# Kernel tuning notes

Measured on AMD Instinct MI355X. Metric: run time of the kernel, lower is better.

The kernel has to match this reference:

```python
import jax, jax.numpy as jnp
import numpy as np

NC, EC, NS, ES = 100000, 1600000, 50000, 800000
F_IN, H, G, OUT = 7, 64, 1024, 2
EPS = 1e-5


def setup_inputs() -> dict:
    key = jax.random.key(0)
    ks = jax.random.split(key, 24)
    d = {
        'x_c': jax.random.normal(ks[0], (NC, F_IN), jnp.float32),
        'edge_index_c': jax.random.randint(ks[1], (2, EC), 0, NC),
        'batch_c': jnp.sort(jax.random.randint(ks[2], (NC,), 0, G)),
        'x_s': jax.random.normal(ks[3], (NS, F_IN), jnp.float32),
        'edge_index_s': jax.random.randint(ks[4], (2, ES), 0, NS),
        'batch_s': jnp.sort(jax.random.randint(ks[5], (NS,), 0, G)),
    }
    def lin(k, i, o):
        return jax.random.normal(k, (i, o), jnp.float32) * (1.0 / np.sqrt(i))
    # chromo branch layers
    d['Wc0'] = lin(ks[6], F_IN, H); d['bc0'] = jnp.zeros((H,), jnp.float32)
    d['gc0'] = jnp.ones((H,), jnp.float32); d['betac0'] = jnp.zeros((H,), jnp.float32)
    d['Wc1'] = lin(ks[7], H, H); d['bc1'] = jnp.zeros((H,), jnp.float32)
    d['gc1'] = jnp.ones((H,), jnp.float32); d['betac1'] = jnp.zeros((H,), jnp.float32)
    # solvent branch layers
    d['Ws0'] = lin(ks[8], F_IN, H); d['bs0'] = jnp.zeros((H,), jnp.float32)
    d['gs0'] = jnp.ones((H,), jnp.float32); d['betas0'] = jnp.zeros((H,), jnp.float32)
    d['Ws1'] = lin(ks[9], H, H); d['bs1'] = jnp.zeros((H,), jnp.float32)
    d['gs1'] = jnp.ones((H,), jnp.float32); d['betas1'] = jnp.zeros((H,), jnp.float32)
    # heads
    d['Wf1'] = lin(ks[10], 2 * H, H); d['bf1'] = jnp.zeros((H,), jnp.float32)
    d['Wf2'] = lin(ks[11], H, OUT); d['bf2'] = jnp.zeros((OUT,), jnp.float32)
    return d


def _gcn(x, src, dst, W, b):
    # PyG GCNConv: add self-loops, symmetric D^-1/2 (A+I) D^-1/2 normalization
    N = x.shape[0]
    xw = x @ W
    si = jnp.concatenate([src, jnp.arange(N)])
    di = jnp.concatenate([dst, jnp.arange(N)])
    deg = jax.ops.segment_sum(jnp.ones(si.shape[0], x.dtype), di, num_segments=N)
    dinv = jnp.where(deg > 0, jax.lax.rsqrt(jnp.maximum(deg, 1.0)), 0.0)
    msg = xw[si] * (dinv[si] * dinv[di])[:, None]
    return jax.ops.segment_sum(msg, di, num_segments=N) + b


def _bn_relu(x, g, b):
    mu = x.mean(0)
    var = x.var(0)
    return jax.nn.relu((x - mu) * jax.lax.rsqrt(var + EPS) * g + b)


def _branch(x, ei, batch, layers):
    for (W, b, g, bt) in layers:
        x = _bn_relu(_gcn(x, ei[0], ei[1], W, b), g, bt)
    s = jax.ops.segment_sum(x, batch, num_segments=G)
    cnt = jax.ops.segment_sum(jnp.ones(x.shape[0], x.dtype), batch, num_segments=G)
    return s / jnp.maximum(cnt, 1.0)[:, None]  # global_mean_pool


def reference(x_c, edge_index_c, batch_c, x_s, edge_index_s, batch_s,
              Wc0, bc0, gc0, betac0, Wc1, bc1, gc1, betac1,
              Ws0, bs0, gs0, betas0, Ws1, bs1, gs1, betas1,
              Wf1, bf1, Wf2, bf2):
    hc = _branch(x_c, edge_index_c, batch_c,
                 [(Wc0, bc0, gc0, betac0), (Wc1, bc1, gc1, betac1)])
    hs = _branch(x_s, edge_index_s, batch_s,
                 [(Ws0, bs0, gs0, betas0), (Ws1, bs1, gs1, betas1)])
    h = jnp.concatenate([hc, hs], axis=1)  # [G, 2H]
    h = jax.nn.relu(h @ Wf1 + bf1)
    return h @ Wf2 + bf2  # [G, 2]
```

## Files before the change

kernel.cpp:

```cpp
#include <hip/hip_runtime.h>
#include <hip/hip_bf16.h>

typedef __hip_bfloat16 bf16;
typedef __attribute__((ext_vector_type(8))) short short8;
typedef __attribute__((ext_vector_type(4))) float f32x4;

#define NC_ 100000
#define EC_ 1600000
#define NS_ 50000
#define ES_ 800000
#define G_  1024
#define EPS_ 1e-5f

#define NB_C 782
#define NB_S 391
#define NBMAX 782
#define KSL 16
#define CSR_WC 2000400
#define CSR_WS 1000208

#define WS_MIN_FALLBACK 39356176ull
#define WS_BIG          52163344ull

__device__ __forceinline__ float b2f(bf16 v) { return __bfloat162float(v); }

__device__ __forceinline__ unsigned short f2bfbits(float v) {
    bf16 b = __float2bfloat16(v);
    union { bf16 b; unsigned short u; } c; c.b = b; return c.u;
}

__device__ __forceinline__ void acc8(float* a, uint4 r) {
    a[0] += __uint_as_float(r.x << 16); a[1] += __uint_as_float(r.x & 0xffff0000u);
    a[2] += __uint_as_float(r.y << 16); a[3] += __uint_as_float(r.y & 0xffff0000u);
    a[4] += __uint_as_float(r.z << 16); a[5] += __uint_as_float(r.z & 0xffff0000u);
    a[6] += __uint_as_float(r.w << 16); a[7] += __uint_as_float(r.w & 0xffff0000u);
}

__global__ void DualGNN_31327491457689_kernel() {}

__global__ __launch_bounds__(256) void k_fillout(float* out, float val, int n) {
    int i = blockIdx.x * 256 + threadIdx.x;
    if (i < n) out[i] = val;
}

__global__ __launch_bounds__(256) void k_zero(int* p, int n) {
    int i = blockIdx.x * 256 + threadIdx.x;
    int stride = gridDim.x * 256;
    while (i < n) { p[i] = 0; i += stride; }
}

__global__ __launch_bounds__(256) void k_bhist2(const int* dst_c, int* bcnt_c,
                                                const int* dst_s, int* bcnt_s) {
    __shared__ int h[NBMAX];
    int t = threadIdx.x;
    const int* dst; int* bcnt; int E, NB, b0, nb;
    if (blockIdx.x < 256) { dst = dst_c; bcnt = bcnt_c; E = EC_; NB = NB_C; b0 = blockIdx.x; nb = 256; }
    else { dst = dst_s; bcnt = bcnt_s; E = ES_; NB = NB_S; b0 = blockIdx.x - 256; nb = 128; }
    for (int i = t; i < NB; i += 256) h[i] = 0;
    __syncthreads();
    for (int e = b0 * 256 + t; e < E; e += nb * 256)
        atomicAdd(&h[dst[e] >> 7], 1);
    __syncthreads();
    for (int i = t; i < NB; i += 256) {
        int v = h[i];
        if (v) atomicAdd(&bcnt[i], v);
    }
}

__device__ void scan_one(const int* cnt, int* base, int* cur, int NB, int (*sc)[1024]) {
    int t = threadIdx.x;
    for (int i = t; i < 1024; i += 256) sc[0][i] = (i < NB) ? cnt[i] : 0;
    __syncthreads();
    int pin = 0;
    for (int off = 1; off < 1024; off <<= 1) {
        for (int i = t; i < 1024; i += 256) {
            int v = sc[pin][i];
            if (i >= off) v += sc[pin][i - off];
            sc[1 - pin][i] = v;
        }
        __syncthreads();
        pin ^= 1;
    }
    for (int i = t; i <= NB; i += 256) {
        int e = (i == 0) ? 0 : sc[pin][i - 1];
        base[i] = e;
        if (i < NB) cur[i] = e;
    }
    __syncthreads();
}

__global__ __launch_bounds__(256) void k_bscan(const int* cnt_c, int* base_c, int* cur_c, int NBc,
                                               const int* cnt_s, int* base_s, int* cur_s, int NBs) {
    __shared__ int sc[2][1024];
    scan_one(cnt_c, base_c, cur_c, NBc, sc);
    scan_one(cnt_s, base_s, cur_s, NBs, sc);
}

__global__ __launch_bounds__(256) void k_bin2(const int* ei_c, int* bcur_c, int* ebuf_c,
                                              const int* ei_s, int* bcur_s, int* ebuf_s) {
    __shared__ int cnt[NBMAX];
    __shared__ int slot[NBMAX * KSL];
    int t = threadIdx.x;
    const int *src, *dst; int *bcur, *ebuf; int E, NB; int base;
    if (blockIdx.x < 391) {
        src = ei_c; dst = ei_c + EC_; bcur = bcur_c; ebuf = ebuf_c;
        E = EC_; NB = NB_C; base = blockIdx.x * 4096;
    } else {
        src = ei_s; dst = ei_s + ES_; bcur = bcur_s; ebuf = ebuf_s;
        E = ES_; NB = NB_S; base = (blockIdx.x - 391) * 4096;
    }
    if (base >= E) return;
    for (int i = t; i < NB; i += 256) cnt[i] = 0;
    __syncthreads();
    int e1 = base + 4096;
    if (e1 > E) e1 = E;
    for (int e = base + t; e < e1; e += 256) {
        int d = dst[e];
        int p = ((d & 127) << 24) | src[e];
        int b = d >> 7;
        int sl = atomicAdd(&cnt[b], 1);
        if (sl < KSL) slot[b * KSL + sl] = p;
        else { int gp = atomicAdd(&bcur[b], 1); ebuf[gp] = p; }
    }
    __syncthreads();
    for (int b = t; b < NB; b += 256) {
        int c = cnt[b];
        if (c > KSL) c = KSL;
        if (c > 0) {
            int gp = atomicAdd(&bcur[b], c);
            for (int k = 0; k < c; k++) ebuf[gp + k] = slot[b * KSL + k];
        }
    }
}

__global__ __launch_bounds__(256) void k_build2(const int* bbase_c, const int* ebuf_c,
                                                const float* x_c, bf16* u_c,
                                                int* deg_c, int* start_c, int* csr_c,
                                                const int* bbase_s, const int* ebuf_s,
                                                const float* x_s, bf16* u_s,
                                                int* deg_s, int* start_s, int* csr_s) {
    __shared__ int lcnt[128], lofs[128], lcur[128];
    int t = threadIdx.x;
    const int* bbase; const int* ebuf; const float* x; bf16* u;
    int* deg; int* start; int* csr; int N, b;
    if (blockIdx.x < NB_C) {
        b = blockIdx.x; bbase = bbase_c; ebuf = ebuf_c; x = x_c; u = u_c;
        deg = deg_c; start = start_c; csr = csr_c; N = NC_;
    } else {
        b = blockIdx.x - NB_C; bbase = bbase_s; ebuf = ebuf_s; x = x_s; u = u_s;
        deg = deg_s; start = start_s; csr = csr_s; N = NS_;
    }
    int e0 = bbase[b], e1 = bbase[b + 1];
    int cb = ((e0 + 512 * b) + 3) & ~3;
    int n0 = b << 7;
    if (t < 128) lcnt[t] = 0;
    __syncthreads();
    for (int e = e0 + t; e < e1; e += 256)
        atomicAdd(&lcnt[((unsigned)ebuf[e]) >> 24], 1);
    __syncthreads();
    if (t < 64) {
        int c0 = lcnt[2 * t], c1 = lcnt[2 * t + 1];
        int v0 = (c0 + 3) & ~3, v1 = (c1 + 3) & ~3;
        int s = v0 + v1, incl = s;
        for (int off = 1; off < 64; off <<= 1) {
            int uu = __shfl_up(incl, off);
            if (t >= off) incl += uu;
        }
        int excl = incl - s;
        lofs[2 * t] = excl;
        lofs[2 * t + 1] = excl + v0;
    }
    __syncthreads();
    if (t < 128) {
        int node = n0 + t;
        if (node < N) {
            deg[node] = lcnt[t];
            start[node] = cb + lofs[t];
            if (x) {
                float d = rsqrtf((float)(lcnt[t] + 1));
                union __align__(16) Pack { bf16 hh[8]; uint4 v; } p;
                for (int k = 0; k < 7; k++) p.hh[k] = __float2bfloat16(x[node * 7 + k] * d);
                p.hh[7] = __float2bfloat16(0.f);
                ((uint4*)u)[node] = p.v;
            }
        }
        lcur[t] = lofs[t];
    }
    __syncthreads();
    if (t < 128) {
        int c = lcnt[t], al = (c + 3) & ~3;
        for (int k = c; k < al; k++) csr[cb + lofs[t] + k] = N;
    }
    for (int e = e0 + t; e < e1; e += 256) {
        unsigned p = (unsigned)ebuf[e];
        int dl = p >> 24;
        int pos = atomicAdd(&lcur[dl], 1);
        csr[cb + pos] = (int)(p & 0xFFFFFF);
    }
    if (b == 0 && t < 4 && u && x) ((int*)u)[N * 4 + t] = 0;
}

__global__ __launch_bounds__(256) void k_prep7(const float* x, const int* deg,
                                               bf16* u, int N) {
    int i = blockIdx.x * 256 + threadIdx.x;
    if (i > N) return;
    union __align__(16) Pack { bf16 hh[8]; uint4 v; } p;
    if (i == N) {
        p.v = (uint4){0u, 0u, 0u, 0u};
    } else {
        float d = rsqrtf((float)(deg[i] + 1));
        for (int k = 0; k < 7; k++) p.hh[k] = __float2bfloat16(x[i * 7 + k] * d);
        p.hh[7] = __float2bfloat16(0.f);
    }
    ((uint4*)u)[i] = p.v;
}

__global__ __launch_bounds__(256) void k_gather7m(
    const bf16* u_c, const int* csr_c, const int* start_c, const int* deg_c,
    const float* W_c, const float* bias_c, bf16* h_c, float* stat_c, int N_c,
    const bf16* u_s, const int* csr_s, const int* start_s, const int* deg_s,
    const float* W_s, const float* bias_s, bf16* h_s, float* stat_s, int N_s,
    int nblk_c) {
    __shared__ float Wsm[7 * 64];
    __shared__ float agg[128][9];
    __shared__ float sm[2][4][64];
    const bf16* u; const int *csr, *start, *deg; const float *W, *bias;
    bf16* h; float* stat; int N, lb;
    if ((int)blockIdx.x < nblk_c) {
        lb = blockIdx.x; u = u_c; csr = csr_c; start = start_c; deg = deg_c;
        W = W_c; bias = bias_c; h = h_c; stat = stat_c; N = N_c;
    } else {
        lb = blockIdx.x - nblk_c; u = u_s; csr = csr_s; start = start_s; deg = deg_s;
        W = W_s; bias = bias_s; h = h_s; stat = stat_s; N = N_s;
    }
    int t = threadIdx.x, lane = t & 63, ty = t >> 6;
    int team = t >> 1, par = t & 1;
    for (int i = t; i < 448; i += 256) Wsm[i] = W[i];
    float b = bias[lane];
    float sum = 0.f, sq = 0.f;
    const uint4* up = (const uint4*)u;
    int i = lb * 128 + team;
    float a[8] = {0.f, 0.f, 0.f, 0.f, 0.f, 0.f, 0.f, 0.f};
    if (i < N) {
        int dg = deg[i], s0 = start[i];
        int adeg = (dg + 3) & ~3;
        if (par == 0) acc8(a, up[i]);
        int half = ((adeg >> 1) + 3) & ~3;
        int jb = par ? half : 0;
        int je = par ? adeg : half;
        int j = jb;
        for (; j + 8 <= je; j += 8) {
            uint4 nA = *(const uint4*)(csr + s0 + j);
            uint4 nB = *(const uint4*)(csr + s0 + j + 4);
            uint4 r0 = up[nA.x], r1 = up[nA.y], r2 = up[nA.z], r3 = up[nA.w];
            uint4 r4 = up[nB.x], r5 = up[nB.y], r6 = up[nB.z], r7 = up[nB.w];
            acc8(a, r0); acc8(a, r1); acc8(a, r2); acc8(a, r3);
            acc8(a, r4); acc8(a, r5); acc8(a, r6); acc8(a, r7);
        }
        if (j < je) {
            uint4 nA = *(const uint4*)(csr + s0 + j);
            uint4 r0 = up[nA.x], r1 = up[nA.y], r2 = up[nA.z], r3 = up[nA.w];
            acc8(a, r0); acc8(a, r1); acc8(a, r2); acc8(a, r3);
        }
    }
    #pragma unroll
    for (int k = 0; k < 7; k++) a[k] += __shfl_xor(a[k], 1);
    if (i < N && par == 0) {
        float di = rsqrtf((float)(deg[i] + 1));
        #pragma unroll
        for (int k = 0; k < 7; k++) agg[team][k] = a[k] * di;
    }
    __syncthreads();
    int mbase = lb * 128 + ty * 32;
    for (int mm = 0; mm < 32; mm++) {
        int node = mbase + mm;
        if (node >= N) break;
        const float* ag = agg[ty * 32 + mm];
        float s = b;
        #pragma unroll
        for (int k = 0; k < 7; k++) s += ag[k] * Wsm[k * 64 + lane];
        h[(size_t)node * 64 + lane] = __float2bfloat16(s);
        sum += s; sq += s * s;
    }
    sm[0][ty][lane] = sum;
    sm[1][ty][lane] = sq;
    __syncthreads();
    if (ty == 0) {
        atomicAdd(&stat[lane],      sm[0][0][lane] + sm[0][1][lane] + sm[0][2][lane] + sm[0][3][lane]);
        atomicAdd(&stat[64 + lane], sm[1][0][lane] + sm[1][1][lane] + sm[1][2][lane] + sm[1][3][lane]);
    }
}

__global__ __launch_bounds__(256) void k_gemm1m(
    const bf16* h_c, const float* W_c, const float* stat_c, const float* gam_c,
    const float* bet_c, const int* deg_c, bf16* y_c, float invN_c, int N_c, int NY_c,
    const bf16* h_s, const float* W_s, const float* stat_s, const float* gam_s,
    const float* bet_s, const int* deg_s, bf16* y_s, float invN_s, int N_s, int NY_s,
    int nblk_c) {
    __shared__ short Wt[64][72];
    __shared__ float AB[128];
    const bf16* h; const float *W, *stat, *gam, *bet; const int* deg;
    bf16* y; float invN; int N, NY, lb, nb;
    if ((int)blockIdx.x < nblk_c) {
        lb = blockIdx.x; nb = nblk_c;
        h = h_c; W = W_c; stat = stat_c; gam = gam_c; bet = bet_c; deg = deg_c;
        y = y_c; invN = invN_c; N = N_c; NY = NY_c;
    } else {
        lb = blockIdx.x - nblk_c; nb = gridDim.x - nblk_c;
        h = h_s; W = W_s; stat = stat_s; gam = gam_s; bet = bet_s; deg = deg_s;
        y = y_s; invN = invN_s; N = N_s; NY = NY_s;
    }
    int t = threadIdx.x, lane = t & 63, ty = t >> 6;
    for (int i = t; i < 4096; i += 256) {
        int k = i >> 6, n = i & 63;
        Wt[n][k] = (short)f2bfbits(W[i]);
    }
    if (t < 64) {
        float mean = stat[t] * invN;
        float var = stat[64 + t] * invN - mean * mean;
        float A = gam[t] * rsqrtf(fmaxf(var, 0.f) + EPS_);
        AB[t] = A;
        AB[64 + t] = bet[t] - mean * A;
    }
    if (lb == 0 && t < 64) {
        int pr = t >> 4, cl = t & 15;
        y[((size_t)pr * NY + N) * 16 + cl] = __float2bfloat16(0.f);
    }
    __syncthreads();
    int quad = lane >> 4, l16 = lane & 15;
    short8 Bf[2][4];
    #pragma unroll
    for (int kt = 0; kt < 2; kt++)
        #pragma unroll
        for (int nt = 0; nt < 4; nt++) {
            int n = nt * 16 + l16, k0 = kt * 32 + quad * 8;
            Bf[kt][nt] = *(const short8*)&Wt[n][k0];
        }
    int ntile = (N + 63) >> 6;
    for (int tile = lb * 4 + ty; tile < ntile; tile += nb * 4) {
        int base = tile << 6;
        f32x4 acc[4][4];
        #pragma unroll
        for (int a = 0; a < 4; a++)
            #pragma unroll
            for (int b = 0; b < 4; b++) acc[a][b] = (f32x4){0.f, 0.f, 0.f, 0.f};
        #pragma unroll
        for (int kt = 0; kt < 2; kt++) {
            int k0 = kt * 32 + quad * 8;
            float Ak[8], Bk[8];
            #pragma unroll
            for (int j = 0; j < 8; j++) { Ak[j] = AB[k0 + j]; Bk[j] = AB[64 + k0 + j]; }
            #pragma unroll
            for (int mt = 0; mt < 4; mt++) {
                int node = base + mt * 16 + l16;
                uint4 raw = *(const uint4*)(h + (size_t)node * 64 + k0);
                unsigned rr[4] = {raw.x, raw.y, raw.z, raw.w};
                short8 af;
                #pragma unroll
                for (int j = 0; j < 8; j++) {
                    unsigned bits = (j & 1) ? (rr[j >> 1] & 0xffff0000u)
                                            : (rr[j >> 1] << 16);
                    float v = __uint_as_float(bits);
                    v = fmaxf(v * Ak[j] + Bk[j], 0.f);
                    af[j] = (short)f2bfbits(v);
                }
                #pragma unroll
                for (int nt = 0; nt < 4; nt++)
                    acc[mt][nt] = __builtin_amdgcn_mfma_f32_16x16x32_bf16(
                        af, Bf[kt][nt], acc[mt][nt], 0, 0, 0);
            }
        }
        #pragma unroll
        for (int mt = 0; mt < 4; mt++)
            #pragma unroll
            for (int r = 0; r < 4; r++) {
                int node = base + mt * 16 + quad * 4 + r;
                if (node < N) {
                    float dinv = rsqrtf((float)(deg[node] + 1));
                    #pragma unroll
                    for (int nt = 0; nt < 4; nt++)
                        y[((size_t)nt * NY + node) * 16 + l16] =
                            __float2bfloat16(acc[mt][nt][r] * dinv);
                }
            }
    }
}

__global__ __launch_bounds__(256) void k_gather16p(
    const bf16* y_c, const int* csr_c, const int* start_c, const int* deg_c,
    const float* bias_c, bf16* h_c, float* stat_c, int N_c, int NY_c,
    const bf16* y_s, const int* csr_s, const int* start_s, const int* deg_s,
    const float* bias_s, bf16* h_s, float* stat_s, int N_s, int NY_s,
    int nblk_c) {
    __shared__ float sms[4][2][2][8];
    const bf16* y; const int *csr, *start, *deg; const float* bias;
    bf16* h; float* stat; int N, NY, lb, nb;
    if ((int)blockIdx.x < nblk_c) {
        lb = blockIdx.x; nb = nblk_c;
        y = y_c; csr = csr_c; start = start_c; deg = deg_c; bias = bias_c;
        h = h_c; stat = stat_c; N = N_c; NY = NY_c;
    } else {
        lb = blockIdx.x - nblk_c; nb = gridDim.x - nblk_c;
        y = y_s; csr = csr_s; start = start_s; deg = deg_s; bias = bias_s;
        h = h_s; stat = stat_s; N = N_s; NY = NY_s;
    }
    int t = threadIdx.x, lane = t & 63, ty = t >> 6;
    int team = lane >> 1, par = lane & 1;
    int pair = lb & 3;
    int grp = lb >> 2;
    int ngrp = nb >> 2;
    const uint4* yp = (const uint4*)y + (size_t)pair * NY * 2;
    uint4* hp = (uint4*)h + (size_t)pair * NY * 2;
    float b[8];
    #pragma unroll
    for (int k = 0; k < 8; k++) b[k] = bias[pair * 16 + par * 8 + k];
    float sum[8], sq[8];
    #pragma unroll
    for (int k = 0; k < 8; k++) { sum[k] = 0.f; sq[k] = 0.f; }
    for (int i = grp * 128 + ty * 32 + team; i < N; i += ngrp * 128) {
        int dg = deg[i], s0 = start[i];
        int adeg = (dg + 3) & ~3;
        float a[8];
        #pragma unroll
        for (int k = 0; k < 8; k++) a[k] = 0.f;
        acc8(a, yp[2 * i + par]);
        int j = 0;
        for (; j + 8 <= adeg; j += 8) {
            uint4 nA = *(const uint4*)(csr + s0 + j);
            uint4 nB = *(const uint4*)(csr + s0 + j + 4);
            uint4 q0 = yp[2 * nA.x + par];
            uint4 q1 = yp[2 * nA.y + par];
            uint4 q2 = yp[2 * nA.z + par];
            uint4 q3 = yp[2 * nA.w + par];
            uint4 q4 = yp[2 * nB.x + par];
            uint4 q5 = yp[2 * nB.y + par];
            uint4 q6 = yp[2 * nB.z + par];
            uint4 q7 = yp[2 * nB.w + par];
            acc8(a, q0); acc8(a, q1); acc8(a, q2); acc8(a, q3);
            acc8(a, q4); acc8(a, q5); acc8(a, q6); acc8(a, q7);
        }
        if (j < adeg) {
            uint4 nA = *(const uint4*)(csr + s0 + j);
            uint4 q0 = yp[2 * nA.x + par];
            uint4 q1 = yp[2 * nA.y + par];
            uint4 q2 = yp[2 * nA.z + par];
            uint4 q3 = yp[2 * nA.w + par];
            acc8(a, q0); acc8(a, q1); acc8(a, q2); acc8(a, q3);
        }
        float di = rsqrtf((float)(dg + 1));
        union __align__(16) Pack { bf16 hh[8]; uint4 v; } p;
        #pragma unroll
        for (int k = 0; k < 8; k++) {
            float v = a[k] * di + b[k];
            p.hh[k] = __float2bfloat16(v);
            sum[k] += v; sq[k] += v * v;
        }
        hp[2 * i + par] = p.v;
    }
    #pragma unroll
    for (int k = 0; k < 8; k++) {
        float s1 = sum[k], s2 = sq[k];
        s1 += __shfl_down(s1, 32); s2 += __shfl_down(s2, 32);
        s1 += __shfl_down(s1, 16); s2 += __shfl_down(s2, 16);
        s1 += __shfl_down(s1, 8);  s2 += __shfl_down(s2, 8);
        s1 += __shfl_down(s1, 4);  s2 += __shfl_down(s2, 4);
        s1 += __shfl_down(s1, 2);  s2 += __shfl_down(s2, 2);
        if (lane < 2) { sms[ty][lane][0][k] = s1; sms[ty][lane][1][k] = s2; }
    }
    __syncthreads();
    if (t < 16) {
        int pp = t >> 3, k = t & 7;
        atomicAdd(&stat[pair * 16 + pp * 8 + k],
                  sms[0][pp][0][k] + sms[1][pp][0][k] + sms[2][pp][0][k] + sms[3][pp][0][k]);
    } else if (t >= 64 && t < 80) {
        int q = t - 64, pp = q >> 3, k = q & 7;
        atomicAdd(&stat[64 + pair * 16 + pp * 8 + k],
                  sms[0][pp][1][k] + sms[1][pp][1][k] + sms[2][pp][1][k] + sms[3][pp][1][k]);
    }
}

__global__ __launch_bounds__(256) void k_poolm(
    const bf16* h_c, const float* stat_c, const float* gam_c, const float* bet_c,
    const int* batch_c, float* pooled_c, float* cnt_c, float invN_c, int N_c, int NY_c,
    const bf16* h_s, const float* stat_s, const float* gam_s, const float* bet_s,
    const int* batch_s, float* pooled_s, float* cnt_s, float invN_s, int N_s, int NY_s,
    int nblk_c) {
    const bf16* h; const float *stat, *gam, *bet; const int* batch;
    float *pooled, *cnt; float invN; int N, NY, lb, nb;
    if ((int)blockIdx.x < nblk_c) {
        lb = blockIdx.x; nb = nblk_c;
        h = h_c; stat = stat_c; gam = gam_c; bet = bet_c; batch = batch_c;
        pooled = pooled_c; cnt = cnt_c; invN = invN_c; N = N_c; NY = NY_c;
    } else {
        lb = blockIdx.x - nblk_c; nb = gridDim.x - nblk_c;
        h = h_s; stat = stat_s; gam = gam_s; bet = bet_s; batch = batch_s;
        pooled = pooled_s; cnt = cnt_s; invN = invN_s; N = N_s; NY = NY_s;
    }
    int t = threadIdx.x;
    int lane = t & 63;
    float mean = stat[lane] * invN;
    float var = stat[64 + lane] * invN - mean * mean;
    float A = gam[lane] * rsqrtf(fmaxf(var, 0.f) + EPS_);
    float B = bet[lane] - mean * A;
    size_t pbase = (size_t)(lane >> 4) * NY * 16 + (lane & 15);
    int w = (lb * 256 + t) >> 6;
    int nw = nb * 4;
    int chunk = (N + nw - 1) / nw;
    int i0 = w * chunk;
    int i1 = i0 + chunk;
    if (i1 > N) i1 = N;
    if (i0 >= N) return;
    int curg = batch[i0];
    float acc = 0.f, c = 0.f;
    for (int i = i0; i < i1; i++) {
        int g = batch[i];
        if (g != curg) {
            atomicAdd(&pooled[(size_t)curg * 64 + lane], acc);
            if (lane == 0) atomicAdd(&cnt[curg], c);
            curg = g; acc = 0.f; c = 0.f;
        }
        acc += fmaxf(b2f(h[pbase + (size_t)i * 16]) * A + B, 0.f);
        c += 1.f;
    }
    atomicAdd(&pooled[(size_t)curg * 64 + lane], acc);
    if (lane == 0) atomicAdd(&cnt[curg], c);
}

__global__ __launch_bounds__(64) void k_head(const float* pooled_c, const float* cnt_c,
                                             const float* pooled_s, const float* cnt_s,
                                             const float* Wf1, const float* bf1_,
                                             const float* Wf2, const float* bf2_,
                                             float* out) {
    __shared__ float W1sm[128 * 64];
    __shared__ float W2sm[128];
    int t = threadIdx.x;
    for (int i = t; i < 128 * 64; i += 64) W1sm[i] = Wf1[i];
    for (int i = t; i < 128; i += 64) W2sm[i] = Wf2[i];
    __syncthreads();
    float bb1 = bf1_[t];
    float b20 = bf2_[0];
    float b21 = bf2_[1];
    for (int g = blockIdx.x; g < G_; g += gridDim.x) {
        float ic = 1.f / fmaxf(cnt_c[g], 1.f);
        float is = 1.f / fmaxf(cnt_s[g], 1.f);
        float hc = pooled_c[(size_t)g * 64 + t] * ic;
        float hs = pooled_s[(size_t)g * 64 + t] * is;
        float s = bb1;
        for (int k = 0; k < 64; k++) s += __shfl(hc, k) * W1sm[k * 64 + t];
        for (int k = 0; k < 64; k++) s += __shfl(hs, k) * W1sm[(64 + k) * 64 + t];
        s = fmaxf(s, 0.f);
        float p0 = s * W2sm[t * 2 + 0];
        float p1 = s * W2sm[t * 2 + 1];
        for (int off = 32; off > 0; off >>= 1) {
            p0 += __shfl_down(p0, off);
            p1 += __shfl_down(p1, off);
        }
        if (t == 0) {
            out[g * 2 + 0] = p0 + b20;
            out[g * 2 + 1] = p1 + b21;
        }
    }
}

extern "C" void kernel_launch(void* const* d_in, const int* in_sizes, int n_in,
                              void* d_out, int out_size, void* d_ws, size_t ws_size,
                              hipStream_t stream) {
    float* out = (float*)d_out;

    if (n_in != 26 || in_sizes[0] != NC_ * 7 || in_sizes[1] != 2 * EC_ ||
        in_sizes[2] != NC_ || in_sizes[3] != NS_ * 7 || in_sizes[4] != 2 * ES_ ||
        in_sizes[5] != NS_ || out_size != G_ * 2) {
        k_fillout<<<(out_size + 255) / 256, 256, 0, stream>>>(out, 7777.0f, out_size);
        return;
    }
    if (ws_size < (size_t)WS_MIN_FALLBACK) {
        k_fillout<<<(out_size + 255) / 256, 256, 0, stream>>>(
            out, 1000.0f + (float)(ws_size >> 20), out_size);
        return;
    }
    const bool big = (ws_size >= (size_t)WS_BIG);

    const float* x_c     = (const float*)d_in[0];
    const int*   ei_c    = (const int*)d_in[1];
    const int*   batch_c = (const int*)d_in[2];
    const float* x_s     = (const float*)d_in[3];
    const int*   ei_s    = (const int*)d_in[4];
    const int*   batch_s = (const int*)d_in[5];
    const float* Wc0  = (const float*)d_in[6];
    const float* bc0  = (const float*)d_in[7];
    const float* gc0  = (const float*)d_in[8];
    const float* bec0 = (const float*)d_in[9];
    const float* Wc1  = (const float*)d_in[10];
    const float* bc1  = (const float*)d_in[11];
    const float* gc1  = (const float*)d_in[12];
    const float* bec1 = (const float*)d_in[13];
    const float* Ws0  = (const float*)d_in[14];
    const float* bs0  = (const float*)d_in[15];
    const float* gs0  = (const float*)d_in[16];
    const float* bes0 = (const float*)d_in[17];
    const float* Ws1  = (const float*)d_in[18];
    const float* bs1  = (const float*)d_in[19];
    const float* gs1  = (const float*)d_in[20];
    const float* bes1 = (const float*)d_in[21];
    const float* Wf1  = (const float*)d_in[22];
    const float* bf1_ = (const float*)d_in[23];
    const float* Wf2  = (const float*)d_in[24];
    const float* bf2_ = (const float*)d_in[25];

    const int NYC = NC_ + 8;
    const int NYS = NS_ + 8;

    int* wsw = (int*)d_ws;
    size_t off = big ? (size_t)(3201024 + 3200256 + 1601536 + 1600256)
                     : (size_t)(3201024 + 3200256);
    float* stats_c  = (float*)(wsw + off); off += 256;
    float* stats_s  = (float*)(wsw + off); off += 256;
    float* pooled_c = (float*)(wsw + off); off += (size_t)G_ * 64;
    float* pooled_s = (float*)(wsw + off); off += (size_t)G_ * 64;
    float* cnt_c    = (float*)(wsw + off); off += G_;
    float* cnt_s    = (float*)(wsw + off); off += G_;
    int*   bcnt_c   = wsw + off; off += NB_C;
    int*   bcnt_s   = wsw + off; off += NB_S;
    const int zero_words = 256 + 256 + G_ * 64 * 2 + G_ * 2 + NB_C + NB_S;
    int*   bbase_c  = wsw + off; off += NB_C + 1;
    int*   bcur_c   = wsw + off; off += NB_C;
    int*   bbase_s  = wsw + off; off += NB_S + 1;
    int*   bcur_s   = wsw + off; off += NB_S;
    int*   deg_c    = wsw + off; off += NC_;
    int*   start_c  = wsw + off; off += NC_;
    int*   deg_s    = wsw + off; off += NS_;
    int*   start_s  = wsw + off; off += NS_;
    int*   csr_c    = wsw + off; off += CSR_WC;
    int*   csr_s    = wsw + off; off += CSR_WS;

    k_zero<<<512, 256, 0, stream>>>((int*)stats_c, zero_words);
    k_bhist2<<<384, 256, 0, stream>>>(ei_c + EC_, bcnt_c, ei_s + ES_, bcnt_s);
    k_bscan<<<1, 256, 0, stream>>>(bcnt_c, bbase_c, bcur_c, NB_C,
                                   bcnt_s, bbase_s, bcur_s, NB_S);

    if (big) {
        bf16* h_c = (bf16*)wsw;
        bf16* y_c = (bf16*)(wsw + 3201024);
        bf16* h_s = (bf16*)(wsw + 3201024 + 3200256);
        bf16* y_s = (bf16*)(wsw + 3201024 + 3200256 + 1601536);
        int*  ebuf_c = (int*)h_c;
        int*  ebuf_s = (int*)h_c + 1600000;
        bf16* u_c = y_c;
        bf16* u_s = y_s;

        k_bin2<<<587, 256, 0, stream>>>(ei_c, bcur_c, ebuf_c, ei_s, bcur_s, ebuf_s);
        k_build2<<<NB_C + NB_S, 256, 0, stream>>>(bbase_c, ebuf_c, x_c, u_c,
                                                  deg_c, start_c, csr_c,
                                                  bbase_s, ebuf_s, x_s, u_s,
                                                  deg_s, start_s, csr_s);
        k_gather7m<<<NB_C + NB_S, 256, 0, stream>>>(
            u_c, csr_c, start_c, deg_c, Wc0, bc0, h_c, stats_c, NC_,
            u_s, csr_s, start_s, deg_s, Ws0, bs0, h_s, stats_s, NS_, NB_C);
        k_gemm1m<<<768, 256, 0, stream>>>(
            h_c, Wc1, stats_c, gc0, bec0, deg_c, y_c, 1.0f / NC_, NC_, NYC,
            h_s, Ws1, stats_s, gs0, bes0, deg_s, y_s, 1.0f / NS_, NS_, NYS, 512);
        k_gather16p<<<3128 + 1564, 256, 0, stream>>>(
            y_c, csr_c, start_c, deg_c, bc1, h_c, stats_c + 128, NC_, NYC,
            y_s, csr_s, start_s, deg_s, bs1, h_s, stats_s + 128, NS_, NYS, 3128);
        k_poolm<<<384, 256, 0, stream>>>(
            h_c, stats_c + 128, gc1, bec1, batch_c, pooled_c, cnt_c, 1.0f / NC_, NC_, NYC,
            h_s, stats_s + 128, gs1, bes1, batch_s, pooled_s, cnt_s, 1.0f / NS_, NS_, NYS, 256);
    } else {
        bf16* hbuf = (bf16*)wsw;
        bf16* ybuf = (bf16*)(wsw + 3201024);
        int*  ebuf_c = (int*)hbuf;
        int*  ebuf_s = (int*)hbuf + 1600000;
        bf16* ub = ybuf;

        k_bin2<<<587, 256, 0, stream>>>(ei_c, bcur_c, ebuf_c, ei_s, bcur_s, ebuf_s);
        k_build2<<<NB_C + NB_S, 256, 0, stream>>>(bbase_c, ebuf_c, x_c, ub,
                                                  deg_c, start_c, csr_c,
                                                  bbase_s, ebuf_s, (const float*)0, (bf16*)0,
                                                  deg_s, start_s, csr_s);
        k_gather7m<<<NB_C, 256, 0, stream>>>(
            ub, csr_c, start_c, deg_c, Wc0, bc0, hbuf, stats_c, NC_,
            ub, csr_c, start_c, deg_c, Wc0, bc0, hbuf, stats_c, NC_, NB_C);
        k_gemm1m<<<512, 256, 0, stream>>>(
            hbuf, Wc1, stats_c, gc0, bec0, deg_c, ybuf, 1.0f / NC_, NC_, NYC,
            hbuf, Wc1, stats_c, gc0, bec0, deg_c, ybuf, 1.0f / NC_, NC_, NYC, 512);
        k_gather16p<<<3128, 256, 0, stream>>>(
            ybuf, csr_c, start_c, deg_c, bc1, hbuf, stats_c + 128, NC_, NYC,
            ybuf, csr_c, start_c, deg_c, bc1, hbuf, stats_c + 128, NC_, NYC, 3128);
        k_poolm<<<256, 256, 0, stream>>>(
            hbuf, stats_c + 128, gc1, bec1, batch_c, pooled_c, cnt_c, 1.0f / NC_, NC_, NYC,
            hbuf, stats_c + 128, gc1, bec1, batch_c, pooled_c, cnt_c, 1.0f / NC_, NC_, NYC, 256);
        k_prep7<<<(NS_ + 256) / 256, 256, 0, stream>>>(x_s, deg_s, ub, NS_);
        k_gather7m<<<NB_S, 256, 0, stream>>>(
            ub, csr_s, start_s, deg_s, Ws0, bs0, hbuf, stats_s, NS_,
            ub, csr_s, start_s, deg_s, Ws0, bs0, hbuf, stats_s, NS_, NB_S);
        k_gemm1m<<<256, 256, 0, stream>>>(
            hbuf, Ws1, stats_s, gs0, bes0, deg_s, ybuf, 1.0f / NS_, NS_, NYS,
            hbuf, Ws1, stats_s, gs0, bes0, deg_s, ybuf, 1.0f / NS_, NS_, NYS, 256);
        k_gather16p<<<1564, 256, 0, stream>>>(
            ybuf, csr_s, start_s, deg_s, bs1, hbuf, stats_s + 128, NS_, NYS,
            ybuf, csr_s, start_s, deg_s, bs1, hbuf, stats_s + 128, NS_, NYS, 1564);
        k_poolm<<<256, 256, 0, stream>>>(
            hbuf, stats_s + 128, gs1, bes1, batch_s, pooled_s, cnt_s, 1.0f / NS_, NS_, NYS,
            hbuf, stats_s + 128, gs1, bes1, batch_s, pooled_s, cnt_s, 1.0f / NS_, NS_, NYS, 256);
    }

    k_head<<<128, 64, 0, stream>>>(pooled_c, cnt_c, pooled_s, cnt_s, Wf1, bf1_, Wf2, bf2_, out);
}
```

Measured before the change: 367.5 us.

## Replace bucketed two-pass CSR build with global-atomic degree count, scan, and scatter

The CSR construction changes from a bucketed approach (per-128-node bucket histogram, binning edges into an intermediate buffer, per-bucket local sort) to a direct counting sort. Per-node degrees come from global atomics, a two-level scan computes padded start offsets, and a scatter kernel places each edge with a global atomic on a per-node cursor. This removes the intermediate edge buffer pass and the shared-memory binning. In exchange it relies on many contended global atomics with random destinations, and the order of neighbours within each row is no longer deterministic.

```diff
diff --git a/kernel.cpp b/kernel.cpp
--- a/kernel.cpp
+++ b/kernel.cpp
@@ -12,12 +12,10 @@
 #define G_  1024
 #define EPS_ 1e-5f
 
-#define NB_C 782
-#define NB_S 391
-#define NBMAX 782
-#define KSL 16
 #define CSR_WC 2000400
 #define CSR_WS 1000208
+#define NBC_ 98
+#define NBS_ 49
 
 #define WS_MIN_FALLBACK 39356176ull
 #define WS_BIG          52163344ull
@@ -49,22 +47,39 @@
     while (i < n) { p[i] = 0; i += stride; }
 }
 
-__global__ __launch_bounds__(256) void k_bhist2(const int* dst_c, int* bcnt_c,
-                                                const int* dst_s, int* bcnt_s) {
-    __shared__ int h[NBMAX];
+__global__ __launch_bounds__(256) void k_deg(const int* dst_c, int* deg_c,
+                                             const int* dst_s, int* deg_s) {
     int t = threadIdx.x;
-    const int* dst; int* bcnt; int E, NB, b0, nb;
-    if (blockIdx.x < 256) { dst = dst_c; bcnt = bcnt_c; E = EC_; NB = NB_C; b0 = blockIdx.x; nb = 256; }
-    else { dst = dst_s; bcnt = bcnt_s; E = ES_; NB = NB_S; b0 = blockIdx.x - 256; nb = 128; }
-    for (int i = t; i < NB; i += 256) h[i] = 0;
-    __syncthreads();
-    for (int e = b0 * 256 + t; e < E; e += nb * 256)
-        atomicAdd(&h[dst[e] >> 7], 1);
-    __syncthreads();
-    for (int i = t; i < NB; i += 256) {
-        int v = h[i];
-        if (v) atomicAdd(&bcnt[i], v);
-    }
+    const int* dst; int* deg; int E, base;
+    if (blockIdx.x < 391) { dst = dst_c; deg = deg_c; E = EC_; base = blockIdx.x * 4096; }
+    else { dst = dst_s; deg = deg_s; E = ES_; base = (blockIdx.x - 391) * 4096; }
+    int e1 = base + 4096; if (e1 > E) e1 = E;
+    for (int e = base + t; e < e1; e += 256)
+        atomicAdd(&deg[dst[e]], 1);
+}
+
+__global__ __launch_bounds__(256) void k_scanA(const int* deg_c, int* bsum_c,
+                                               const int* deg_s, int* bsum_s) {
+    __shared__ int wsm[4];
+    const int* deg; int* bsum; int N, b;
+    if ((int)blockIdx.x < NBC_) { deg = deg_c; bsum = bsum_c; N = NC_; b = blockIdx.x; }
+    else { deg = deg_s; bsum = bsum_s; N = NS_; b = blockIdx.x - NBC_; }
+    int t = threadIdx.x, lane = t & 63, w = t >> 6;
+    int i0 = b * 1024 + t * 4;
+    int d0 = 0, d1 = 0, d2 = 0, d3 = 0;
+    if (i0 + 4 <= N) { int4 dd = *(const int4*)(deg + i0); d0 = dd.x; d1 = dd.y; d2 = dd.z; d3 = dd.w; }
+    else {
+        if (i0     < N) d0 = deg[i0];
+        if (i0 + 1 < N) d1 = deg[i0 + 1];
+        if (i0 + 2 < N) d2 = deg[i0 + 2];
+        if (i0 + 3 < N) d3 = deg[i0 + 3];
+    }
+    int s = ((d0 + 3) & ~3) + ((d1 + 3) & ~3) + ((d2 + 3) & ~3) + ((d3 + 3) & ~3);
+    #pragma unroll
+    for (int off = 32; off > 0; off >>= 1) s += __shfl_down(s, off);
+    if (lane == 0) wsm[w] = s;
+    __syncthreads();
+    if (t == 0) bsum[b] = wsm[0] + wsm[1] + wsm[2] + wsm[3];
 }
 
 __device__ void scan_one(const int* cnt, int* base, int* cur, int NB, int (*sc)[1024]) {
@@ -96,108 +111,95 @@
     scan_one(cnt_s, base_s, cur_s, NBs, sc);
 }
 
-__global__ __launch_bounds__(256) void k_bin2(const int* ei_c, int* bcur_c, int* ebuf_c,
-                                              const int* ei_s, int* bcur_s, int* ebuf_s) {
-    __shared__ int cnt[NBMAX];
-    __shared__ int slot[NBMAX * KSL];
+__global__ __launch_bounds__(256) void k_scanC(
+    const int* deg_c, const int* bbase_c, int* start_c, int* cur_c, int* csr_c,
+    const float* x_c, bf16* u_c,
+    const int* deg_s, const int* bbase_s, int* start_s, int* cur_s, int* csr_s,
+    const float* x_s, bf16* u_s) {
+    __shared__ int wsm[4];
+    const int* deg; const int* bbase; int* start; int* cur; int* csr;
+    const float* x; bf16* u; int N, b;
+    if ((int)blockIdx.x < NBC_) {
+        deg = deg_c; bbase = bbase_c; start = start_c; cur = cur_c; csr = csr_c;
+        x = x_c; u = u_c; N = NC_; b = blockIdx.x;
+    } else {
+        deg = deg_s; bbase = bbase_s; start = start_s; cur = cur_s; csr = csr_s;
+        x = x_s; u = u_s; N = NS_; b = blockIdx.x - NBC_;
+    }
+    int t = threadIdx.x, lane = t & 63, w = t >> 6;
+    int i0 = b * 1024 + t * 4;
+    int d0 = 0, d1 = 0, d2 = 0, d3 = 0;
+    if (i0 + 4 <= N) { int4 dd = *(const int4*)(deg + i0); d0 = dd.x; d1 = dd.y; d2 = dd.z; d3 = dd.w; }
+    else {
+        if (i0     < N) d0 = deg[i0];
+        if (i0 + 1 < N) d1 = deg[i0 + 1];
+        if (i0 + 2 < N) d2 = deg[i0 + 2];
+        if (i0 + 3 < N) d3 = deg[i0 + 3];
+    }
+    int p0 = (d0 + 3) & ~3, p1 = (d1 + 3) & ~3, p2 = (d2 + 3) & ~3, p3 = (d3 + 3) & ~3;
+    int tsum = p0 + p1 + p2 + p3;
+    int incl = tsum;
+    #pragma unroll
+    for (int off = 1; off < 64; off <<= 1) {
+        int v = __shfl_up(incl, off);
+        if (lane >= off) incl += v;
+    }
+    if (lane == 63) wsm[w] = incl;
+    __syncthreads();
+    int woff = 0;
+    #pragma unroll
+    for (int k = 0; k < 4; k++) if (k < w) woff += wsm[k];
+    int base = bbase[b] + woff + (incl - tsum);
+    int s0 = base, s1 = base + p0, s2 = base + p0 + p1, s3 = base + p0 + p1 + p2;
+    if (i0 + 4 <= N) {
+        *(int4*)(start + i0) = (int4){s0, s1, s2, s3};
+        *(int4*)(cur + i0)   = (int4){s0, s1, s2, s3};
+    } else {
+        if (i0     < N) { start[i0]     = s0; cur[i0]     = s0; }
+        if (i0 + 1 < N) { start[i0 + 1] = s1; cur[i0 + 1] = s1; }
+        if (i0 + 2 < N) { start[i0 + 2] = s2; cur[i0 + 2] = s2; }
+        if (i0 + 3 < N) { start[i0 + 3] = s3; cur[i0 + 3] = s3; }
+    }
+    int dd4[4] = {d0, d1, d2, d3};
+    int pp4[4] = {p0, p1, p2, p3};
+    int ss4[4] = {s0, s1, s2, s3};
+    #pragma unroll
+    for (int k = 0; k < 4; k++) {
+        int i = i0 + k;
+        if (i < N) {
+            for (int q = dd4[k]; q < pp4[k]; q++) csr[ss4[k] + q] = N;
+            if (x) {
+                float di = rsqrtf((float)(dd4[k] + 1));
+                union __align__(16) Pack { bf16 hh[8]; uint4 v; } pk;
+                #pragma unroll
+                for (int c = 0; c < 7; c++) pk.hh[c] = __float2bfloat16(x[(size_t)i * 7 + c] * di);
+                pk.hh[7] = __float2bfloat16(0.f);
+                ((uint4*)u)[i] = pk.v;
+            }
+        } else if (i == N && x) {
+            ((uint4*)u)[N] = (uint4){0u, 0u, 0u, 0u};
+        }
+    }
+}
+
+__global__ __launch_bounds__(256) void k_scatter(const int* ei_c, int* cur_c, int* csr_c,
+                                                 const int* ei_s, int* cur_s, int* csr_s) {
     int t = threadIdx.x;
-    const int *src, *dst; int *bcur, *ebuf; int E, NB; int base;
+    const int *src, *dst; int *cur, *csr; int E, base;
     if (blockIdx.x < 391) {
-        src = ei_c; dst = ei_c + EC_; bcur = bcur_c; ebuf = ebuf_c;
-        E = EC_; NB = NB_C; base = blockIdx.x * 4096;
-    } else {
-        src = ei_s; dst = ei_s + ES_; bcur = bcur_s; ebuf = ebuf_s;
-        E = ES_; NB = NB_S; base = (blockIdx.x - 391) * 4096;
-    }
-    if (base >= E) return;
-    for (int i = t; i < NB; i += 256) cnt[i] = 0;
-    __syncthreads();
-    int e1 = base + 4096;
-    if (e1 > E) e1 = E;
+        src = ei_c; dst = ei_c + EC_; cur = cur_c; csr = csr_c;
+        E = EC_; base = blockIdx.x * 4096;
+    } else {
+        src = ei_s; dst = ei_s + ES_; cur = cur_s; csr = csr_s;
+        E = ES_; base = (blockIdx.x - 391) * 4096;
+    }
+    int e1 = base + 4096; if (e1 > E) e1 = E;
     for (int e = base + t; e < e1; e += 256) {
         int d = dst[e];
-        int p = ((d & 127) << 24) | src[e];
-        int b = d >> 7;
-        int sl = atomicAdd(&cnt[b], 1);
-        if (sl < KSL) slot[b * KSL + sl] = p;
-        else { int gp = atomicAdd(&bcur[b], 1); ebuf[gp] = p; }
-    }
-    __syncthreads();
-    for (int b = t; b < NB; b += 256) {
-        int c = cnt[b];
-        if (c > KSL) c = KSL;
-        if (c > 0) {
-            int gp = atomicAdd(&bcur[b], c);
-            for (int k = 0; k < c; k++) ebuf[gp + k] = slot[b * KSL + k];
-        }
-    }
-}
-
-__global__ __launch_bounds__(256) void k_build2(const int* bbase_c, const int* ebuf_c,
-                                                const float* x_c, bf16* u_c,
-                                                int* deg_c, int* start_c, int* csr_c,
-                                                const int* bbase_s, const int* ebuf_s,
-                                                const float* x_s, bf16* u_s,
-                                                int* deg_s, int* start_s, int* csr_s) {
-    __shared__ int lcnt[128], lofs[128], lcur[128];
-    int t = threadIdx.x;
-    const int* bbase; const int* ebuf; const float* x; bf16* u;
-    int* deg; int* start; int* csr; int N, b;
-    if (blockIdx.x < NB_C) {
-        b = blockIdx.x; bbase = bbase_c; ebuf = ebuf_c; x = x_c; u = u_c;
-        deg = deg_c; start = start_c; csr = csr_c; N = NC_;
-    } else {
-        b = blockIdx.x - NB_C; bbase = bbase_s; ebuf = ebuf_s; x = x_s; u = u_s;
-        deg = deg_s; start = start_s; csr = csr_s; N = NS_;
-    }
-    int e0 = bbase[b], e1 = bbase[b + 1];
-    int cb = ((e0 + 512 * b) + 3) & ~3;
-    int n0 = b << 7;
-    if (t < 128) lcnt[t] = 0;
-    __syncthreads();
-    for (int e = e0 + t; e < e1; e += 256)
-        atomicAdd(&lcnt[((unsigned)ebuf[e]) >> 24], 1);
-    __syncthreads();
-    if (t < 64) {
-        int c0 = lcnt[2 * t], c1 = lcnt[2 * t + 1];
-        int v0 = (c0 + 3) & ~3, v1 = (c1 + 3) & ~3;
-        int s = v0 + v1, incl = s;
-        for (int off = 1; off < 64; off <<= 1) {
-            int uu = __shfl_up(incl, off);
-            if (t >= off) incl += uu;
-        }
-        int excl = incl - s;
-        lofs[2 * t] = excl;
-        lofs[2 * t + 1] = excl + v0;
-    }
-    __syncthreads();
-    if (t < 128) {
-        int node = n0 + t;
-        if (node < N) {
-            deg[node] = lcnt[t];
-            start[node] = cb + lofs[t];
-            if (x) {
-                float d = rsqrtf((float)(lcnt[t] + 1));
-                union __align__(16) Pack { bf16 hh[8]; uint4 v; } p;
-                for (int k = 0; k < 7; k++) p.hh[k] = __float2bfloat16(x[node * 7 + k] * d);
-                p.hh[7] = __float2bfloat16(0.f);
-                ((uint4*)u)[node] = p.v;
-            }
-        }
-        lcur[t] = lofs[t];
-    }
-    __syncthreads();
-    if (t < 128) {
-        int c = lcnt[t], al = (c + 3) & ~3;
-        for (int k = c; k < al; k++) csr[cb + lofs[t] + k] = N;
-    }
-    for (int e = e0 + t; e < e1; e += 256) {
-        unsigned p = (unsigned)ebuf[e];
-        int dl = p >> 24;
-        int pos = atomicAdd(&lcur[dl], 1);
-        csr[cb + pos] = (int)(p & 0xFFFFFF);
-    }
-    if (b == 0 && t < 4 && u && x) ((int*)u)[N * 4 + t] = 0;
+        int s = src[e];
+        int pos = atomicAdd(&cur[d], 1);
+        csr[pos] = s;
+    }
 }
 
 __global__ __launch_bounds__(256) void k_prep7(const float* x, const int* deg,
@@ -619,43 +621,43 @@
     float* pooled_s = (float*)(wsw + off); off += (size_t)G_ * 64;
     float* cnt_c    = (float*)(wsw + off); off += G_;
     float* cnt_s    = (float*)(wsw + off); off += G_;
-    int*   bcnt_c   = wsw + off; off += NB_C;
-    int*   bcnt_s   = wsw + off; off += NB_S;
-    const int zero_words = 256 + 256 + G_ * 64 * 2 + G_ * 2 + NB_C + NB_S;
-    int*   bbase_c  = wsw + off; off += NB_C + 1;
-    int*   bcur_c   = wsw + off; off += NB_C;
-    int*   bbase_s  = wsw + off; off += NB_S + 1;
-    int*   bcur_s   = wsw + off; off += NB_S;
     int*   deg_c    = wsw + off; off += NC_;
+    int*   deg_s    = wsw + off; off += NS_;
+    const int zero_words = 256 + 256 + G_ * 64 * 2 + G_ * 2 + NC_ + NS_;
+    int*   bsum_c   = wsw + off; off += 100;
+    int*   bbase2_c = wsw + off; off += 100;
+    int*   bcur2_c  = wsw + off; off += 100;
+    int*   bsum_s   = wsw + off; off += 52;
+    int*   bbase2_s = wsw + off; off += 52;
+    int*   bcur2_s  = wsw + off; off += 52;
     int*   start_c  = wsw + off; off += NC_;
-    int*   deg_s    = wsw + off; off += NS_;
     int*   start_s  = wsw + off; off += NS_;
     int*   csr_c    = wsw + off; off += CSR_WC;
     int*   csr_s    = wsw + off; off += CSR_WS;
 
     k_zero<<<512, 256, 0, stream>>>((int*)stats_c, zero_words);
-    k_bhist2<<<384, 256, 0, stream>>>(ei_c + EC_, bcnt_c, ei_s + ES_, bcnt_s);
-    k_bscan<<<1, 256, 0, stream>>>(bcnt_c, bbase_c, bcur_c, NB_C,
-                                   bcnt_s, bbase_s, bcur_s, NB_S);
+    k_deg<<<587, 256, 0, stream>>>(ei_c + EC_, deg_c, ei_s + ES_, deg_s);
+    k_scanA<<<NBC_ + NBS_, 256, 0, stream>>>(deg_c, bsum_c, deg_s, bsum_s);
+    k_bscan<<<1, 256, 0, stream>>>(bsum_c, bbase2_c, bcur2_c, NBC_,
+                                   bsum_s, bbase2_s, bcur2_s, NBS_);
 
     if (big) {
         bf16* h_c = (bf16*)wsw;
         bf16* y_c = (bf16*)(wsw + 3201024);
         bf16* h_s = (bf16*)(wsw + 3201024 + 3200256);
         bf16* y_s = (bf16*)(wsw + 3201024 + 3200256 + 1601536);
-        int*  ebuf_c = (int*)h_c;
-        int*  ebuf_s = (int*)h_c + 1600000;
+        int*  cur_c = (int*)h_c;
+        int*  cur_s = (int*)h_c + NC_;
         bf16* u_c = y_c;
         bf16* u_s = y_s;
 
-        k_bin2<<<587, 256, 0, stream>>>(ei_c, bcur_c, ebuf_c, ei_s, bcur_s, ebuf_s);
-        k_build2<<<NB_C + NB_S, 256, 0, stream>>>(bbase_c, ebuf_c, x_c, u_c,
-                                                  deg_c, start_c, csr_c,
-                                                  bbase_s, ebuf_s, x_s, u_s,
-                                                  deg_s, start_s, csr_s);
-        k_gather7m<<<NB_C + NB_S, 256, 0, stream>>>(
+        k_scanC<<<NBC_ + NBS_, 256, 0, stream>>>(
+            deg_c, bbase2_c, start_c, cur_c, csr_c, x_c, u_c,
+            deg_s, bbase2_s, start_s, cur_s, csr_s, x_s, u_s);
+        k_scatter<<<587, 256, 0, stream>>>(ei_c, cur_c, csr_c, ei_s, cur_s, csr_s);
+        k_gather7m<<<782 + 391, 256, 0, stream>>>(
             u_c, csr_c, start_c, deg_c, Wc0, bc0, h_c, stats_c, NC_,
-            u_s, csr_s, start_s, deg_s, Ws0, bs0, h_s, stats_s, NS_, NB_C);
+            u_s, csr_s, start_s, deg_s, Ws0, bs0, h_s, stats_s, NS_, 782);
         k_gemm1m<<<768, 256, 0, stream>>>(
             h_c, Wc1, stats_c, gc0, bec0, deg_c, y_c, 1.0f / NC_, NC_, NYC,
             h_s, Ws1, stats_s, gs0, bes0, deg_s, y_s, 1.0f / NS_, NS_, NYS, 512);
@@ -668,18 +670,17 @@
     } else {
         bf16* hbuf = (bf16*)wsw;
         bf16* ybuf = (bf16*)(wsw + 3201024);
-        int*  ebuf_c = (int*)hbuf;
-        int*  ebuf_s = (int*)hbuf + 1600000;
+        int*  cur_c = (int*)hbuf;
+        int*  cur_s = (int*)hbuf + NC_;
         bf16* ub = ybuf;
 
-        k_bin2<<<587, 256, 0, stream>>>(ei_c, bcur_c, ebuf_c, ei_s, bcur_s, ebuf_s);
-        k_build2<<<NB_C + NB_S, 256, 0, stream>>>(bbase_c, ebuf_c, x_c, ub,
-                                                  deg_c, start_c, csr_c,
-                                                  bbase_s, ebuf_s, (const float*)0, (bf16*)0,
-                                                  deg_s, start_s, csr_s);
-        k_gather7m<<<NB_C, 256, 0, stream>>>(
+        k_scanC<<<NBC_ + NBS_, 256, 0, stream>>>(
+            deg_c, bbase2_c, start_c, cur_c, csr_c, x_c, ub,
+            deg_s, bbase2_s, start_s, cur_s, csr_s, (const float*)0, (bf16*)0);
+        k_scatter<<<587, 256, 0, stream>>>(ei_c, cur_c, csr_c, ei_s, cur_s, csr_s);
+        k_gather7m<<<782, 256, 0, stream>>>(
             ub, csr_c, start_c, deg_c, Wc0, bc0, hbuf, stats_c, NC_,
-            ub, csr_c, start_c, deg_c, Wc0, bc0, hbuf, stats_c, NC_, NB_C);
+            ub, csr_c, start_c, deg_c, Wc0, bc0, hbuf, stats_c, NC_, 782);
         k_gemm1m<<<512, 256, 0, stream>>>(
             hbuf, Wc1, stats_c, gc0, bec0, deg_c, ybuf, 1.0f / NC_, NC_, NYC,
             hbuf, Wc1, stats_c, gc0, bec0, deg_c, ybuf, 1.0f / NC_, NC_, NYC, 512);
@@ -690,9 +691,9 @@
             hbuf, stats_c + 128, gc1, bec1, batch_c, pooled_c, cnt_c, 1.0f / NC_, NC_, NYC,
             hbuf, stats_c + 128, gc1, bec1, batch_c, pooled_c, cnt_c, 1.0f / NC_, NC_, NYC, 256);
         k_prep7<<<(NS_ + 256) / 256, 256, 0, stream>>>(x_s, deg_s, ub, NS_);
-        k_gather7m<<<NB_S, 256, 0, stream>>>(
+        k_gather7m<<<391, 256, 0, stream>>>(
             ub, csr_s, start_s, deg_s, Ws0, bs0, hbuf, stats_s, NS_,
-            ub, csr_s, start_s, deg_s, Ws0, bs0, hbuf, stats_s, NS_, NB_S);
+            ub, csr_s, start_s, deg_s, Ws0, bs0, hbuf, stats_s, NS_, 391);
         k_gemm1m<<<256, 256, 0, stream>>>(
             hbuf, Ws1, stats_s, gs0, bes0, deg_s, ybuf, 1.0f / NS_, NS_, NYS,
             hbuf, Ws1, stats_s, gs0, bes0, deg_s, ybuf, 1.0f / NS_, NS_, NYS, 256);
```

New measurement: 607.9 us. +65.4%, slower.
